# Kernel tuning notes

Measured on AMD Instinct MI355X. Metric: run time of the kernel, lower is better.

## Reference

```python
import jax, jax.numpy as jnp
import numpy as np

B, C, IMG_H, IMG_W = 64, 3, 640, 640
PH, PW = 128, 128


def setup_inputs() -> dict:
    key = jax.random.key(0)
    k1, k2, k3, k4, k5, k6 = jax.random.split(key, 6)
    images = jax.random.uniform(k1, (B, C, IMG_H, IMG_W), jnp.float32)
    patch = jax.random.uniform(k2, (C, PH, PW), jnp.float32)
    # torch.randint(-30, 30) and 0.8 + 0.4*rand equivalents
    angles = jax.random.randint(k3, (B,), -30, 30).astype(jnp.float32)
    scales = 0.8 + 0.4 * jax.random.uniform(k4, (B,), jnp.float32)
    ux = jax.random.uniform(k5, (B,), jnp.float32)  # -> x_location = floor(ux * max_x)
    uy = jax.random.uniform(k6, (B,), jnp.float32)
    return {"images": images, "patch": patch, "angles": angles,
            "scales": scales, "ux": ux, "uy": uy}


def _bilinear(patch, yp, xp):
    """Bilinear sample patch (C,ph,pw) at float coords yp,xp (B,H,W); OOB -> 0."""
    Cc, ph, pw = patch.shape
    y0 = jnp.floor(yp)
    x0 = jnp.floor(xp)
    wy = yp - y0
    wx = xp - x0

    def g(yi, xi):
        inb = (yi >= 0) & (yi <= ph - 1) & (xi >= 0) & (xi <= pw - 1)
        yc = jnp.clip(yi, 0, ph - 1).astype(jnp.int32)
        xc = jnp.clip(xi, 0, pw - 1).astype(jnp.int32)
        return patch[:, yc, xc] * inb.astype(patch.dtype)[None]  # (C,B,H,W)

    out = (g(y0, x0) * ((1 - wy) * (1 - wx))[None]
           + g(y0, x0 + 1) * ((1 - wy) * wx)[None]
           + g(y0 + 1, x0) * (wy * (1 - wx))[None]
           + g(y0 + 1, x0 + 1) * (wy * wx)[None])
    return out


def reference(images, patch, angles, scales, ux, uy):
    b, c, H, W = images.shape
    ph, pw = patch.shape[1], patch.shape[2]
    dt = images.dtype

    sh = jnp.floor(ph * scales)            # scaled patch height, (B,)
    sw = jnp.floor(pw * scales)
    y0 = jnp.floor(uy * (H - sh))          # paste top-left, (B,)
    x0 = jnp.floor(ux * (W - sw))

    yy = jnp.arange(H, dtype=dt)[None, :, None]   # (1,H,1)
    xx = jnp.arange(W, dtype=dt)[None, None, :]   # (1,1,W)
    yl = yy - y0[:, None, None]            # coords inside paste rect, (B,H,W)
    xl = xx - x0[:, None, None]
    valid = (yl >= 0) & (yl < sh[:, None, None]) & (xl >= 0) & (xl < sw[:, None, None])

    # inverse of resize (scaled -> rotated patch coords, align_corners=False)
    yr = (yl + 0.5) * (ph / sh)[:, None, None] - 0.5
    xr = (xl + 0.5) * (pw / sw)[:, None, None] - 0.5

    # inverse of CCW rotation about patch center (angles in degrees)
    theta = jnp.deg2rad(angles)[:, None, None]
    cy = (ph - 1) / 2.0
    cx = (pw - 1) / 2.0
    dy = yr - cy
    dx = xr - cx
    co = jnp.cos(theta)
    si = jnp.sin(theta)
    xp = co * dx + si * dy + cx
    yp = -si * dx + co * dy + cy

    samp = jnp.transpose(_bilinear(patch, yp, xp), (1, 0, 2, 3))  # (B,C,H,W)
    return jnp.where(valid[:, None], samp, images)
```

## Files before the change

kernel.cpp:

```cpp
#include <hip/hip_runtime.h>

#define BB   64
#define CCH  3
#define HH   640
#define WW   640
#define PHH  128
#define PWW  128

__global__ __launch_bounds__(256) void patch_apply_kernel(
    const float* __restrict__ images,
    const float* __restrict__ patch,
    const float* __restrict__ angles,
    const float* __restrict__ scales,
    const float* __restrict__ ux,
    const float* __restrict__ uy,
    float* __restrict__ out)
{
    const int QW = WW / 4;
    int idx = blockIdx.x * blockDim.x + threadIdx.x;
    int b   = idx / (HH * QW);
    int rem = idx - b * (HH * QW);
    int y   = rem / QW;
    int x   = (rem - y * QW) * 4;

    const size_t plane = (size_t)HH * WW;
    const size_t base  = (size_t)b * CCH * plane + (size_t)y * WW + x;

    float4 v0 = *(const float4*)(images + base);
    float4 v1 = *(const float4*)(images + base + plane);
    float4 v2 = *(const float4*)(images + base + 2 * plane);

    float scale = scales[b];
    float sh  = floorf((float)PHH * scale);
    float sw  = floorf((float)PWW * scale);
    float y0f = floorf(uy[b] * ((float)HH - sh));
    float x0f = floorf(ux[b] * ((float)WW - sw));

    float yl  = (float)y - y0f;
    float xl0 = (float)x - x0f;

    bool rowv = (yl >= 0.0f) && (yl < sh);
    bool anyx = (xl0 + 3.0f >= 0.0f) && (xl0 < sw);

    if (rowv && anyx) {
        float theta = angles[b] * 0.017453292519943295f;
        float si, co;
        sincosf(theta, &si, &co);
        float rh = (float)PHH / sh;
        float rw = (float)PWW / sw;
        const float cy = (PHH - 1) * 0.5f;
        const float cx = (PWW - 1) * 0.5f;

        float yr = (yl + 0.5f) * rh - 0.5f;
        float dy = yr - cy;

        #pragma unroll
        for (int j = 0; j < 4; ++j) {
            float xl = xl0 + (float)j;
            if (xl >= 0.0f && xl < sw) {
                float xr = (xl + 0.5f) * rw - 0.5f;
                float dx = xr - cx;
                float xp = co * dx + si * dy + cx;
                float yp = -si * dx + co * dy + cy;

                float yfl = floorf(yp);
                float xfl = floorf(xp);
                float wy = yp - yfl;
                float wx = xp - xfl;
                int yi = (int)yfl;
                int xi = (int)xfl;

                bool iy0 = (yi     >= 0) && (yi     <= PHH - 1);
                bool iy1 = (yi + 1 >= 0) && (yi + 1 <= PHH - 1);
                bool ix0 = (xi     >= 0) && (xi     <= PWW - 1);
                bool ix1 = (xi + 1 >= 0) && (xi + 1 <= PWW - 1);

                int yc0 = min(max(yi,     0), PHH - 1);
                int yc1 = min(max(yi + 1, 0), PHH - 1);
                int xc0 = min(max(xi,     0), PWW - 1);
                int xc1 = min(max(xi + 1, 0), PWW - 1);

                float w00 = ((1.0f - wy) * (1.0f - wx)) * ((iy0 && ix0) ? 1.0f : 0.0f);
                float w01 = ((1.0f - wy) * wx)          * ((iy0 && ix1) ? 1.0f : 0.0f);
                float w10 = (wy * (1.0f - wx))          * ((iy1 && ix0) ? 1.0f : 0.0f);
                float w11 = (wy * wx)                   * ((iy1 && ix1) ? 1.0f : 0.0f);

                int o00 = yc0 * PWW + xc0;
                int o01 = yc0 * PWW + xc1;
                int o10 = yc1 * PWW + xc0;
                int o11 = yc1 * PWW + xc1;

                #pragma unroll
                for (int c = 0; c < 3; ++c) {
                    const float* p = patch + c * (PHH * PWW);
                    float s = p[o00] * w00 + p[o01] * w01
                            + p[o10] * w10 + p[o11] * w11;
                    if (c == 0)      ((float*)&v0)[j] = s;
                    else if (c == 1) ((float*)&v1)[j] = s;
                    else             ((float*)&v2)[j] = s;
                }
            }
        }
    }

    *(float4*)(out + base)             = v0;
    *(float4*)(out + base + plane)     = v1;
    *(float4*)(out + base + 2 * plane) = v2;
}

extern "C" void kernel_launch(void* const* d_in, const int* in_sizes, int n_in,
                              void* d_out, int out_size, void* d_ws, size_t ws_size,
                              hipStream_t stream) {
    const float* images = (const float*)d_in[0];
    const float* patch  = (const float*)d_in[1];
    const float* angles = (const float*)d_in[2];
    const float* scales = (const float*)d_in[3];
    const float* ux     = (const float*)d_in[4];
    const float* uy     = (const float*)d_in[5];
    float* out = (float*)d_out;

    const int total  = BB * HH * (WW / 4);
    const int block  = 256;
    const int blocks = total / block;
    patch_apply_kernel<<<blocks, block, 0, stream>>>(
        images, patch, angles, scales, ux, uy, out);
}
```

Measured before the change: 500.0 us.

## Split into bulk image copy kernel plus a separate patch-rect paste kernel

Replaces the fused per-pixel kernel with a plain float4 copy of images into the output, followed by a second kernel launched only over the scaled patch rectangle of each image, which computes the bilinear samples and overwrites those pixels. This takes the per-pixel coordinate and validity math off most of the image and makes the bulk pass a simple streaming copy. In exchange it adds a second launch and rewrites patch pixels after they were already copied, and the paste kernel uses scalar, partly unaligned stores.

After: 509.8 us. Within noise of the previous version (+2.0%).

```diff
diff --git a/kernel.cpp b/kernel.cpp
--- a/kernel.cpp
+++ b/kernel.cpp
@@ -7,8 +7,15 @@
 #define PHH  128
 #define PWW  128
 
-__global__ __launch_bounds__(256) void patch_apply_kernel(
-    const float* __restrict__ images,
+__global__ __launch_bounds__(256) void copy_kernel(
+    const float4* __restrict__ src,
+    float4* __restrict__ dst)
+{
+    size_t i = (size_t)blockIdx.x * 256 + threadIdx.x;
+    dst[i] = src[i];
+}
+
+__global__ __launch_bounds__(192) void patch_paste_kernel(
     const float* __restrict__ patch,
     const float* __restrict__ angles,
     const float* __restrict__ scales,
@@ -16,96 +23,76 @@
     const float* __restrict__ uy,
     float* __restrict__ out)
 {
-    const int QW = WW / 4;
-    int idx = blockIdx.x * blockDim.x + threadIdx.x;
-    int b   = idx / (HH * QW);
-    int rem = idx - b * (HH * QW);
-    int y   = rem / QW;
-    int x   = (rem - y * QW) * 4;
+    const int b  = blockIdx.y;
+    const int yy = blockIdx.x;
+    const int xx = threadIdx.x;
+
+    const float scale = scales[b];
+    const float sh = floorf((float)PHH * scale);
+    const float sw = floorf((float)PWW * scale);
+
+    if ((float)yy >= sh) return;
+    if ((float)xx >= sw) return;
+
+    const float y0f = floorf(uy[b] * ((float)HH - sh));
+    const float x0f = floorf(ux[b] * ((float)WW - sw));
+    const int y0i = (int)y0f;
+    const int x0i = (int)x0f;
+
+    const float theta = angles[b] * 0.017453292519943295f;
+    float si, co;
+    sincosf(theta, &si, &co);
+    const float rh = (float)PHH / sh;
+    const float rw = (float)PWW / sw;
+    const float cy = (PHH - 1) * 0.5f;
+    const float cx = (PWW - 1) * 0.5f;
+
+    const float yr = ((float)yy + 0.5f) * rh - 0.5f;
+    const float xr = ((float)xx + 0.5f) * rw - 0.5f;
+    const float dy = yr - cy;
+    const float dx = xr - cx;
+
+    const float xp = co * dx + si * dy + cx;
+    const float yp = -si * dx + co * dy + cy;
+
+    const float yfl = floorf(yp);
+    const float xfl = floorf(xp);
+    const float wy = yp - yfl;
+    const float wx = xp - xfl;
+    const int yi = (int)yfl;
+    const int xi = (int)xfl;
+
+    const bool iy0 = (yi     >= 0) && (yi     <= PHH - 1);
+    const bool iy1 = (yi + 1 >= 0) && (yi + 1 <= PHH - 1);
+    const bool ix0 = (xi     >= 0) && (xi     <= PWW - 1);
+    const bool ix1 = (xi + 1 >= 0) && (xi + 1 <= PWW - 1);
+
+    const int yc0 = min(max(yi,     0), PHH - 1);
+    const int yc1 = min(max(yi + 1, 0), PHH - 1);
+    const int xc0 = min(max(xi,     0), PWW - 1);
+    const int xc1 = min(max(xi + 1, 0), PWW - 1);
+
+    const float w00 = ((1.0f - wy) * (1.0f - wx)) * ((iy0 && ix0) ? 1.0f : 0.0f);
+    const float w01 = ((1.0f - wy) * wx)          * ((iy0 && ix1) ? 1.0f : 0.0f);
+    const float w10 = (wy * (1.0f - wx))          * ((iy1 && ix0) ? 1.0f : 0.0f);
+    const float w11 = (wy * wx)                   * ((iy1 && ix1) ? 1.0f : 0.0f);
+
+    const int o00 = yc0 * PWW + xc0;
+    const int o01 = yc0 * PWW + xc1;
+    const int o10 = yc1 * PWW + xc0;
+    const int o11 = yc1 * PWW + xc1;
 
     const size_t plane = (size_t)HH * WW;
-    const size_t base  = (size_t)b * CCH * plane + (size_t)y * WW + x;
+    const size_t base  = (size_t)b * CCH * plane
+                       + (size_t)(y0i + yy) * WW + (x0i + xx);
 
-    float4 v0 = *(const float4*)(images + base);
-    float4 v1 = *(const float4*)(images + base + plane);
-    float4 v2 = *(const float4*)(images + base + 2 * plane);
-
-    float scale = scales[b];
-    float sh  = floorf((float)PHH * scale);
-    float sw  = floorf((float)PWW * scale);
-    float y0f = floorf(uy[b] * ((float)HH - sh));
-    float x0f = floorf(ux[b] * ((float)WW - sw));
-
-    float yl  = (float)y - y0f;
-    float xl0 = (float)x - x0f;
-
-    bool rowv = (yl >= 0.0f) && (yl < sh);
-    bool anyx = (xl0 + 3.0f >= 0.0f) && (xl0 < sw);
-
-    if (rowv && anyx) {
-        float theta = angles[b] * 0.017453292519943295f;
-        float si, co;
-        sincosf(theta, &si, &co);
-        float rh = (float)PHH / sh;
-        float rw = (float)PWW / sw;
-        const float cy = (PHH - 1) * 0.5f;
-        const float cx = (PWW - 1) * 0.5f;
-
-        float yr = (yl + 0.5f) * rh - 0.5f;
-        float dy = yr - cy;
-
-        #pragma unroll
-        for (int j = 0; j < 4; ++j) {
-            float xl = xl0 + (float)j;
-            if (xl >= 0.0f && xl < sw) {
-                float xr = (xl + 0.5f) * rw - 0.5f;
-                float dx = xr - cx;
-                float xp = co * dx + si * dy + cx;
-                float yp = -si * dx + co * dy + cy;
-
-                float yfl = floorf(yp);
-                float xfl = floorf(xp);
-                float wy = yp - yfl;
-                float wx = xp - xfl;
-                int yi = (int)yfl;
-                int xi = (int)xfl;
-
-                bool iy0 = (yi     >= 0) && (yi     <= PHH - 1);
-                bool iy1 = (yi + 1 >= 0) && (yi + 1 <= PHH - 1);
-                bool ix0 = (xi     >= 0) && (xi     <= PWW - 1);
-                bool ix1 = (xi + 1 >= 0) && (xi + 1 <= PWW - 1);
-
-                int yc0 = min(max(yi,     0), PHH - 1);
-                int yc1 = min(max(yi + 1, 0), PHH - 1);
-                int xc0 = min(max(xi,     0), PWW - 1);
-                int xc1 = min(max(xi + 1, 0), PWW - 1);
-
-                float w00 = ((1.0f - wy) * (1.0f - wx)) * ((iy0 && ix0) ? 1.0f : 0.0f);
-                float w01 = ((1.0f - wy) * wx)          * ((iy0 && ix1) ? 1.0f : 0.0f);
-                float w10 = (wy * (1.0f - wx))          * ((iy1 && ix0) ? 1.0f : 0.0f);
-                float w11 = (wy * wx)                   * ((iy1 && ix1) ? 1.0f : 0.0f);
-
-                int o00 = yc0 * PWW + xc0;
-                int o01 = yc0 * PWW + xc1;
-                int o10 = yc1 * PWW + xc0;
-                int o11 = yc1 * PWW + xc1;
-
-                #pragma unroll
-                for (int c = 0; c < 3; ++c) {
-                    const float* p = patch + c * (PHH * PWW);
-                    float s = p[o00] * w00 + p[o01] * w01
-                            + p[o10] * w10 + p[o11] * w11;
-                    if (c == 0)      ((float*)&v0)[j] = s;
-                    else if (c == 1) ((float*)&v1)[j] = s;
-                    else             ((float*)&v2)[j] = s;
-                }
-            }
-        }
+    #pragma unroll
+    for (int c = 0; c < 3; ++c) {
+        const float* p = patch + c * (PHH * PWW);
+        float s = p[o00] * w00 + p[o01] * w01
+                + p[o10] * w10 + p[o11] * w11;
+        out[base + (size_t)c * plane] = s;
     }
-
-    *(float4*)(out + base)             = v0;
-    *(float4*)(out + base + plane)     = v1;
-    *(float4*)(out + base + 2 * plane) = v2;
 }
 
 extern "C" void kernel_launch(void* const* d_in, const int* in_sizes, int n_in,
@@ -119,9 +106,12 @@
     const float* uy     = (const float*)d_in[5];
     float* out = (float*)d_out;
 
-    const int total  = BB * HH * (WW / 4);
-    const int block  = 256;
-    const int blocks = total / block;
-    patch_apply_kernel<<<blocks, block, 0, stream>>>(
-        images, patch, angles, scales, ux, uy, out);
+    const int n_f4    = BB * CCH * HH * WW / 4;
+    const int cblocks = n_f4 / 256;
+    copy_kernel<<<cblocks, 256, 0, stream>>>(
+        (const float4*)images, (float4*)out);
+
+    dim3 pgrid(154, BB);
+    patch_paste_kernel<<<pgrid, 192, 0, stream>>>(
+        patch, angles, scales, ux, uy, out);
 }
```
